# Kernel optimization log

Measured on AMD Instinct MI355X. Metric: run time of the kernel, lower is better.

The kernel has to match this reference:

```python
import jax, jax.numpy as jnp
import numpy as np

# Geometry constants hardcoded in the torch module
B, H, W = 1, 256, 256
A, DC = 64, 1024            # n_views, det_count
NSAMP = 512                  # samples per ray for the line integral
DSRC, DDET, SPACING = 500.0, 500.0, 2.0
NPAD = 2048                  # fft padding (next pow2 >= 2*DC)
FEAT = 32


def _bilinear_image(img, px, py):
    """Bilinear sample img (B,H,W) at centered coords px,py (any shape). Zero outside."""
    b, hh, ww = img.shape
    cx = px + (ww - 1) / 2.0
    cy = py + (hh - 1) / 2.0
    x0 = jnp.floor(cx); y0 = jnp.floor(cy)
    fx = cx - x0; fy = cy - y0
    x0i = x0.astype(jnp.int32); y0i = y0.astype(jnp.int32)
    flat = img.reshape(b, -1)

    def gather(yi, xi):
        valid = (yi >= 0) & (yi < hh) & (xi >= 0) & (xi < ww)
        yc = jnp.clip(yi, 0, hh - 1); xc = jnp.clip(xi, 0, ww - 1)
        idx = (yc * ww + xc).reshape(-1)
        v = jnp.take(flat, idx, axis=1).reshape((b,) + yi.shape)
        return v * valid.astype(img.dtype)

    return (gather(y0i, x0i) * (1 - fx) * (1 - fy)
            + gather(y0i, x0i + 1) * fx * (1 - fy)
            + gather(y0i + 1, x0i) * (1 - fx) * fy
            + gather(y0i + 1, x0i + 1) * fx * fy)


def fan_forward(img, theta):
    """Ray-driven fan-beam forward projection. img (B,1,H,W) -> sino (B,A,DC)."""
    im = img[:, 0]
    c = jnp.cos(theta); s = jnp.sin(theta)
    src = DSRC * jnp.stack([c, s], -1)                    # (A,2) source positions
    e = jnp.stack([-s, c], -1)                            # detector axis
    u = (jnp.arange(DC) - (DC - 1) / 2.0) * SPACING       # detector offsets
    det = -DDET * jnp.stack([c, s], -1)[:, None, :] + u[None, :, None] * e[:, None, :]  # (A,DC,2)
    d = det - src[:, None, :]
    L = jnp.sqrt(jnp.sum(d * d, axis=-1))                 # (A,DC) ray lengths
    t = (jnp.arange(NSAMP, dtype=jnp.float32) + 0.5) / NSAMP
    pts = src[:, None, None, :] + t[None, None, :, None] * d[:, :, None, :]  # (A,DC,N,2)
    vals = _bilinear_image(im, pts[..., 0], pts[..., 1])  # (B,A,DC,N)
    return jnp.sum(vals, axis=-1) * (L / NSAMP)[None]


def filter_sinogram(sino):
    """Ram-Lak ramp filtering along the detector axis with zero-padding."""
    f = jnp.abs(jnp.fft.rfftfreq(NPAD)).astype(jnp.float32)  # cycles/sample
    sf = jnp.fft.rfft(sino, n=NPAD, axis=-1) * (2.0 * f)
    return jnp.fft.irfft(sf, n=NPAD, axis=-1)[..., :DC].astype(sino.dtype)


def fan_backprojection(sino, theta):
    """Pixel-driven fan-beam backprojection. sino (B,A,DC) -> (B,1,H,W)."""
    xs = jnp.arange(W, dtype=jnp.float32) - (W - 1) / 2.0
    ys = jnp.arange(H, dtype=jnp.float32) - (H - 1) / 2.0
    gx, gy = jnp.meshgrid(xs, ys)                         # (H,W)
    c = jnp.cos(theta)[:, None, None]; s = jnp.sin(theta)[:, None, None]
    xr = gx[None] * c + gy[None] * s                      # (A,H,W) rotated coords
    yr = -gx[None] * s + gy[None] * c
    denom = DSRC - xr
    uu = yr * (DSRC + DDET) / denom                       # detector coordinate
    wgt = (DSRC * DSRC) / (denom * denom)                 # fan-beam distance weight
    iu = uu / SPACING + (DC - 1) / 2.0
    i0 = jnp.floor(iu); fr = iu - i0
    i0i = i0.astype(jnp.int32)
    aidx = jnp.arange(A)[:, None, None]
    b = sino.shape[0]
    flat = sino.reshape(b, -1)

    def g(ii):
        valid = (ii >= 0) & (ii < DC)
        ic = jnp.clip(ii, 0, DC - 1)
        idx = (aidx * DC + ic).reshape(-1)
        v = jnp.take(flat, idx, axis=1).reshape((b, A, H, W))
        return v * valid.astype(sino.dtype)

    vals = g(i0i) * (1 - fr) + g(i0i + 1) * fr            # (B,A,H,W)
    bp = jnp.sum(vals * wgt[None], axis=1) * (jnp.pi / A)
    return bp[:, None]


def conv(x, w):
    return jax.lax.conv_general_dilated(x, w, (1, 1), 'SAME',
                                        dimension_numbers=('NCHW', 'OIHW', 'NCHW'))


def setup_inputs():
    key = jax.random.key(0)
    ks = jax.random.split(key, 8)
    x = jax.random.normal(ks[0], (B, 1, H, W), jnp.float32)
    theta = jnp.arange(A, dtype=jnp.float32) * (2.0 * np.pi / A)
    sinogram = jax.random.normal(ks[1], (B, A, DC), jnp.float32)

    def xav(k, shape):
        fan_in = shape[1] * 9; fan_out = shape[0] * 9
        return jax.random.normal(k, shape, jnp.float32) * np.sqrt(2.0 / (fan_in + fan_out)).astype(np.float32)

    return {
        'x': x, 'theta': theta, 'sinogram': sinogram,
        'lambda_step': jnp.float32(0.5), 'soft_thr': jnp.float32(0.01),
        'conv1_forward': xav(ks[2], (FEAT, 1, 3, 3)),
        'conv2_forward': xav(ks[3], (FEAT, FEAT, 3, 3)),
        'conv1_backward': xav(ks[4], (FEAT, FEAT, 3, 3)),
        'conv2_backward': xav(ks[5], (1, FEAT, 3, 3)),
    }


def reference(x, theta, sinogram, lambda_step, soft_thr,
              conv1_forward, conv2_forward, conv1_backward, conv2_backward):
    sino_pred = fan_forward(x, theta)
    filtered = filter_sinogram(sino_pred)
    X_fbp = fan_backprojection(filtered - sinogram, theta)
    x_input = x - lambda_step * X_fbp
    h = jax.nn.relu(conv(x_input, conv1_forward))
    x_forward = conv(h, conv2_forward)
    hs = jnp.sign(x_forward) * jax.nn.relu(jnp.abs(x_forward) - soft_thr)
    x_pred = conv(jax.nn.relu(conv(hs, conv1_backward)), conv2_backward)
    x_est = conv(jax.nn.relu(conv(x_forward, conv1_backward)), conv2_backward)
    symloss = x_est - x_input
    return (x_pred, symloss)
```

## Files before the change

### kernel.cpp

```cpp
#include <hip/hip_runtime.h>

#define DEV_INLINE __device__ __forceinline__

#define PI_F 3.14159265358979323846f

#define H_OFF     0
#define SINO_OFF  2048
#define DIFF_OFF  67584
#define XIN_OFF   133120
#define WF2F_OFF  198656
#define WF1B_OFF  207872
#define WF2B_OFF  212480
#define BUFA_OFF  217088
#define BUFB_OFF  2314240

typedef short bf16x8 __attribute__((ext_vector_type(8)));
typedef float f32x4 __attribute__((ext_vector_type(4)));

union FragI4 { int4 i4; bf16x8 v; };
union I4U    { int4 i4; int i[4]; };

DEV_INLINE unsigned rne1(float a) {
  unsigned u = __float_as_uint(a);
  return (u + 0x7FFFu + ((u >> 16) & 1u)) >> 16;
}
DEV_INLINE int pack_rne(float a, float b) {
  return (int)(rne1(a) | (rne1(b) << 16));
}

__global__ __launch_bounds__(256) void setup_kernel(
    const float* __restrict__ sino_in, const float* __restrict__ w2f,
    const float* __restrict__ w1b, const float* __restrict__ w2b,
    const float* __restrict__ img,
    float* __restrict__ h, float* __restrict__ diff,
    int* __restrict__ wf2f, int* __restrict__ wf1b, int* __restrict__ wf2b,
    float4* __restrict__ quadP, float* __restrict__ x_input) {
  const int b = blockIdx.x;
  const int tid = threadIdx.x;
  if (b < 64) {
    __shared__ float hp[8][32];
    const int cell = tid & 31;
    const int kq = tid >> 5;
    const int n = b * 32 + cell;
    float ssum = 0.0f;
    const float ang_scale = PI_F / 1024.0f;
    for (int k = kq * 128; k < kq * 128 + 128; ++k) {
      int m = (k * n) & 2047;
      ssum += (float)k * __cosf((float)m * ang_scale);
    }
    hp[kq][cell] = ssum;
    __syncthreads();
    if (tid < 32) {
      float S = 0.0f;
      #pragma unroll
      for (int q = 0; q < 8; ++q) S += hp[q][tid];
      int nn = b * 32 + tid;
      float sgn = (nn & 1) ? -1.0f : 1.0f;
      h[nn] = (S * (1.0f / 512.0f) + sgn) * (1.0f / 2048.0f);
    }
  } else if (b < 320) {
    int idx = (b - 64) * 256 + tid;
    diff[idx] = -sino_in[idx];
  } else if (b < 356) {
    const bool second = (b >= 338);
    int idx = (b - (second ? 338 : 320)) * 256 + tid;
    int d = idx & 3;
    int L = (idx >> 2) & 63;
    int jm = idx >> 8;
    int j = jm >> 1, mt = jm & 1;
    int co = mt * 16 + (L & 15);
    int ci0 = (L >> 4) * 8 + 2 * d;
    const float* w = second ? w1b : w2f;
    int v = pack_rne(w[co * 288 + ci0 * 9 + j], w[co * 288 + (ci0 + 1) * 9 + j]);
    (second ? wf1b : wf2f)[idx] = v;
  } else if (b < 617) {
    int idx = (b - 356) * 256 + tid;
    if (idx < 258 * 258) {
      int y = idx / 258;
      int x = idx - y * 258;
      float4 v;
      int ay = y - 1, bx = x - 1;
      bool y0ok = (ay >= 0 && ay < 256);
      bool y1ok = (ay + 1 >= 0 && ay + 1 < 256);
      bool x0ok = (bx >= 0 && bx < 256);
      bool x1ok = (bx + 1 >= 0 && bx + 1 < 256);
      v.x = (y0ok && x0ok) ? img[(ay << 8) + bx] : 0.0f;
      v.y = (y0ok && x1ok) ? img[(ay << 8) + bx + 1] : 0.0f;
      v.z = (y1ok && x0ok) ? img[((ay + 1) << 8) + bx] : 0.0f;
      v.w = (y1ok && x1ok) ? img[((ay + 1) << 8) + bx + 1] : 0.0f;
      quadP[idx] = v;
    }
  } else if (b < 873) {
    int idx = (b - 617) * 256 + tid;
    x_input[idx] = img[idx];
  } else {
    int d = tid & 3;
    int L = tid >> 2;
    int n = L & 15;
    int k0 = (L >> 4) * 8 + 2 * d;
    float lo = (n < 9) ? w2b[k0 * 9 + n] : 0.0f;
    float hi = (n < 9) ? w2b[(k0 + 1) * 9 + n] : 0.0f;
    wf2b[tid] = pack_rne(lo, hi);
  }
}

__global__ __launch_bounds__(256) void fwdproj(
    const float4* __restrict__ quadP, const float* __restrict__ theta,
    float* __restrict__ sino) {
  __shared__ float part[8][32];
  __shared__ float cs[2];
  const int tid = threadIdx.x;
  const int a = blockIdx.x >> 5;
  const int cell = tid & 31;
  const int chunk = tid >> 5;
  const int d = ((blockIdx.x & 31) << 5) + cell;
  if (tid == 0) {
    float th = theta[a];
    cs[0] = cosf(th);
    cs[1] = sinf(th);
  }
  __syncthreads();
  const float c = cs[0], s = cs[1];
  const float u = ((float)d - 511.5f) * 2.0f;
  const float dxv = -1000.0f * c - u * s;
  const float dyv = -1000.0f * s + u * c;
  const float L = sqrtf(1.0e6f + u * u);
  const float sx = fmaf(500.0f, c, 127.5f);
  const float sy = fmaf(500.0f, s, 127.5f);

  float tlo = 0.0f, thi = 1.0f;
  if (fabsf(dxv) > 1e-6f) {
    float inv = 1.0f / dxv;
    float a0 = (-1.0f - sx) * inv, a1 = (256.0f - sx) * inv;
    tlo = fmaxf(tlo, fminf(a0, a1));
    thi = fminf(thi, fmaxf(a0, a1));
  } else if (sx <= -1.0f || sx >= 256.0f) {
    thi = -1.0f;
  }
  if (fabsf(dyv) > 1e-6f) {
    float inv = 1.0f / dyv;
    float a0 = (-1.0f - sy) * inv, a1 = (256.0f - sy) * inv;
    tlo = fmaxf(tlo, fminf(a0, a1));
    thi = fminf(thi, fmaxf(a0, a1));
  } else if (sy <= -1.0f || sy >= 256.0f) {
    thi = -1.0f;
  }
  int imin = (int)ceilf(tlo * 512.0f - 0.5f) - 1;
  imin = imin < 0 ? 0 : imin;
  int imax = (int)floorf(thi * 512.0f - 0.5f) + 1;
  imax = imax > 511 ? 511 : imax;

  float acc = 0.0f;
  for (int i = imin + chunk; i <= imax; i += 8) {
    float t = ((float)i + 0.5f) * (1.0f / 512.0f);
    float cx = fmaf(t, dxv, sx);
    float cy = fmaf(t, dyv, sy);
    cx = fminf(fmaxf(cx, -1.0f), 256.0f);
    cy = fminf(fmaxf(cy, -1.0f), 256.0f);
    float xf = floorf(cx), yf = floorf(cy);
    float fx = cx - xf, fy = cy - yf;
    int ix = (int)xf + 1;
    int iy = (int)yf + 1;
    float4 q = quadP[iy * 258 + ix];
    float gx = 1.0f - fx, gy = 1.0f - fy;
    acc += gy * (gx * q.x + fx * q.y) + fy * (gx * q.z + fx * q.w);
  }
  part[chunk][cell] = acc;
  __syncthreads();
  if (tid < 32) {
    float r = 0.0f;
    #pragma unroll
    for (int q = 0; q < 8; ++q) r += part[q][tid];
    sino[a * 1024 + ((blockIdx.x & 31) << 5) + tid] = r * (L * (1.0f / 512.0f));
  }
}

__global__ __launch_bounds__(256) void filt(
    const float* __restrict__ sino_pred, const float* __restrict__ h,
    float* __restrict__ diff) {
  __shared__ __align__(16) float srow[256];
  __shared__ __align__(16) float hext[4104];
  const int a = blockIdx.x >> 2;
  const int q = blockIdx.x & 3;
  const int tid = threadIdx.x;
  const int k0base = q * 256;
  srow[tid] = sino_pred[a * 1024 + k0base + tid];
  for (int n = tid; n < 4104; n += 256) hext[n] = h[(n - 2051) & 2047];
  __syncthreads();
  const int dd0 = tid * 4;
  float acc0 = 0.f, acc1 = 0.f, acc2 = 0.f, acc3 = 0.f;
  #pragma unroll 4
  for (int kk = 0; kk < 256; kk += 4) {
    float4 sv = *reinterpret_cast<const float4*>(&srow[kk]);
    int nb = dd0 + 2048 - k0base - kk;
    float4 hA = *reinterpret_cast<const float4*>(&hext[nb]);
    float4 hB = *reinterpret_cast<const float4*>(&hext[nb + 4]);
    acc0 = fmaf(sv.x, hA.w, acc0); acc0 = fmaf(sv.y, hA.z, acc0);
    acc0 = fmaf(sv.z, hA.y, acc0); acc0 = fmaf(sv.w, hA.x, acc0);
    acc1 = fmaf(sv.x, hB.x, acc1); acc1 = fmaf(sv.y, hA.w, acc1);
    acc1 = fmaf(sv.z, hA.z, acc1); acc1 = fmaf(sv.w, hA.y, acc1);
    acc2 = fmaf(sv.x, hB.y, acc2); acc2 = fmaf(sv.y, hB.x, acc2);
    acc2 = fmaf(sv.z, hA.w, acc2); acc2 = fmaf(sv.w, hA.z, acc2);
    acc3 = fmaf(sv.x, hB.z, acc3); acc3 = fmaf(sv.y, hB.y, acc3);
    acc3 = fmaf(sv.z, hB.x, acc3); acc3 = fmaf(sv.w, hA.w, acc3);
  }
  float* o = diff + a * 1024 + dd0;
  atomicAdd(o + 0, acc0);
  atomicAdd(o + 1, acc1);
  atomicAdd(o + 2, acc2);
  atomicAdd(o + 3, acc3);
}

__global__ __launch_bounds__(256) void backproj_part(
    const float* __restrict__ diff, const float* __restrict__ theta,
    const float* __restrict__ lam_p, float* __restrict__ x_input) {
  __shared__ float cst[16], snt[16];
  const int tid = threadIdx.x;
  const int tileb = blockIdx.x & 255;
  const int a0 = (blockIdx.x >> 8) << 4;
  if (tid < 16) {
    float th = theta[a0 + tid];
    cst[tid] = cosf(th);
    snt[tid] = sinf(th);
  }
  __syncthreads();
  const int tX = (tileb & 3) << 6;
  const int tY = (tileb >> 2) << 2;
  const int pxi = tX + (tid & 63);
  const int pyi = tY + (tid >> 6);
  const float gx = (float)pxi - 127.5f;
  const float gy = (float)pyi - 127.5f;
  float acc = 0.0f;
  for (int ai = 0; ai < 16; ++ai) {
    float c = cst[ai], s = snt[ai];
    float xr = gx * c + gy * s;
    float yr = gy * c - gx * s;
    float denom = 500.0f - xr;
    float inv = 1.0f / denom;
    float uu = yr * 1000.0f * inv;
    float wgt = 250000.0f * inv * inv;
    float iu = uu * 0.5f + 511.5f;
    float i0f = floorf(iu);
    float fr = iu - i0f;
    int i0 = (int)i0f;
    int c0 = min(max(i0, 0), 1023);
    int c1 = min(max(i0 + 1, 0), 1023);
    float m0 = (i0 >= 0 && i0 < 1024) ? 1.0f : 0.0f;
    float m1 = (i0 + 1 >= 0 && i0 + 1 < 1024) ? 1.0f : 0.0f;
    const float* row = diff + (a0 + ai) * 1024;
    float v0 = row[c0] * m0;
    float v1 = row[c1] * m1;
    acc += (v0 * (1.0f - fr) + v1 * fr) * wgt;
  }
  int p = (pyi << 8) + pxi;
  atomicAdd(x_input + p, -lam_p[0] * 0.04908738521234052f * acc);
}

__global__ __launch_bounds__(256) void conv12f(
    const float* __restrict__ x_input, const float* __restrict__ w1f,
    const int* __restrict__ wf2f, int* __restrict__ xfp) {
  __shared__ float xin[8][36];
  __shared__ __align__(16) int htile[3264];
  const int tid = threadIdx.x;
  const int lane = tid & 63;
  const int wave = tid >> 6;
  const int tX = (blockIdx.x & 7) << 5;
  const int tY = (blockIdx.x >> 3) << 2;

  FragI4 wf[2][9];
  const int4* wfg = (const int4*)wf2f;
  #pragma unroll
  for (int mt = 0; mt < 2; ++mt)
    #pragma unroll
    for (int j = 0; j < 9; ++j) wf[mt][j].i4 = wfg[(j * 2 + mt) * 64 + lane];

  for (int idx = tid; idx < 288; idx += 256) {
    int sy = idx / 36;
    int sx = idx - sy * 36;
    int gy = tY + sy - 2, gx = tX + sx - 2;
    xin[sy][sx] = (gy >= 0 && gy < 256 && gx >= 0 && gx < 256)
                      ? x_input[(gy << 8) + gx] : 0.0f;
  }
  __syncthreads();

  for (int pos = tid; pos < 204; pos += 256) {
    int yy = pos / 34;
    int xx = pos - yy * 34;
    int hy = tY + yy - 1, hx = tX + xx - 1;
    bool hin = (hy >= 0 && hy < 256 && hx >= 0 && hx < 256);
    float v[9];
    #pragma unroll
    for (int dy = 0; dy < 3; ++dy)
      #pragma unroll
      for (int dx = 0; dx < 3; ++dx) v[dy * 3 + dx] = xin[yy + dy][xx + dx];
    int packs[16];
    #pragma unroll
    for (int c2 = 0; c2 < 16; ++c2) {
      float r0 = 0.0f, r1 = 0.0f;
      #pragma unroll
      for (int j = 0; j < 9; ++j) {
        r0 = fmaf(v[j], w1f[(2 * c2) * 9 + j], r0);
        r1 = fmaf(v[j], w1f[(2 * c2 + 1) * 9 + j], r1);
      }
      r0 = hin ? fmaxf(r0, 0.0f) : 0.0f;
      r1 = hin ? fmaxf(r1, 0.0f) : 0.0f;
      packs[c2] = pack_rne(r0, r1);
    }
    #pragma unroll
    for (int g = 0; g < 4; ++g)
      *reinterpret_cast<int4*>(&htile[g * 816 + pos * 4]) =
          make_int4(packs[4 * g], packs[4 * g + 1],
                    packs[4 * g + 2], packs[4 * g + 3]);
  }
  __syncthreads();

  const int y = wave;
  const int n = lane & 15;
  const int q = lane >> 4;
  const int qb = q * 816;
  for (int xt = 0; xt < 2; ++xt) {
    const int x0 = xt << 4;
    f32x4 acc0 = {0.f, 0.f, 0.f, 0.f};
    f32x4 acc1 = {0.f, 0.f, 0.f, 0.f};
    #pragma unroll
    for (int j = 0; j < 9; ++j) {
      int dy = j / 3, dx = j - dy * 3;
      int pb = (y + dy) * 34 + x0 + dx + n;
      FragI4 bf;
      bf.i4 = *reinterpret_cast<const int4*>(&htile[qb + pb * 4]);
      acc0 = __builtin_amdgcn_mfma_f32_16x16x32_bf16(wf[0][j].v, bf.v, acc0, 0, 0, 0);
      acc1 = __builtin_amdgcn_mfma_f32_16x16x32_bf16(wf[1][j].v, bf.v, acc1, 0, 0, 0);
    }
    const int gpos = ((tY + y) << 8) + tX + x0 + n;
    int2* xp = (int2*)(xfp + (gpos << 4));
    xp[q]     = make_int2(pack_rne(acc0[0], acc0[1]), pack_rne(acc0[2], acc0[3]));
    xp[4 + q] = make_int2(pack_rne(acc1[0], acc1[1]), pack_rne(acc1[2], acc1[3]));
  }
}

__global__ __launch_bounds__(256) void branch_tail(
    const int* __restrict__ xfp, const int* __restrict__ wf1b,
    const int* __restrict__ wf2b, const float* __restrict__ thr_p,
    const float* __restrict__ x_input, float* __restrict__ out) {
  __shared__ __align__(16) int ldsX[8704];
  __shared__ __align__(16) int ldsD[6400];
  float* ldsP = (float*)ldsX;
  const int tid = threadIdx.x;
  const int lane = tid & 63;
  const int wave = tid >> 6;
  const int branch = blockIdx.x >> 8;
  const int tileb = blockIdx.x & 255;
  const int tX = (tileb & 3) << 6;
  const int tY = (tileb >> 2) << 2;
  const float thr = thr_p[0];
  const bool soft = (branch == 0);

  FragI4 wf[2][9];
  const int4* wfg = (const int4*)wf1b;
  #pragma unroll
  for (int mt = 0; mt < 2; ++mt)
    #pragma unroll
    for (int j = 0; j < 9; ++j) wf[mt][j].i4 = wfg[(j * 2 + mt) * 64 + lane];
  FragI4 wb;
  wb.i4 = ((const int4*)wf2b)[lane];

  if (tid < 16) {
    int g = tid >> 2, px = 396 + (tid & 3);
    *reinterpret_cast<int4*>(&ldsD[g * 1600 + px * 4]) = make_int4(0, 0, 0, 0);
  }

  #pragma unroll
  for (int t = 0; t < 3; ++t) {
    int p = tid + t * 256;
    if (p < 544) {
      int sy = p / 68;
      int sx = p - sy * 68;
      int gy = tY + sy - 2, gx = tX + sx - 2;
      bool ok = ((unsigned)gy < 256u) && ((unsigned)gx < 256u);
      I4U w[4];
      if (ok) {
        const int4* src = (const int4*)(xfp + (((gy << 8) + gx) << 4));
        w[0].i4 = src[0]; w[1].i4 = src[1]; w[2].i4 = src[2]; w[3].i4 = src[3];
      } else {
        w[0].i4 = w[1].i4 = w[2].i4 = w[3].i4 = make_int4(0, 0, 0, 0);
      }
      #pragma unroll
      for (int g = 0; g < 4; ++g) {
        if (soft) {
          #pragma unroll
          for (int k = 0; k < 4; ++k) {
            int v = w[g].i[k];
            float lo = __uint_as_float(((unsigned)v) << 16);
            float hi = __uint_as_float(((unsigned)v) & 0xFFFF0000u);
            lo = fmaxf(lo - thr, 0.0f) + fminf(lo + thr, 0.0f);
            hi = fmaxf(hi - thr, 0.0f) + fminf(hi + thr, 0.0f);
            w[g].i[k] = pack_rne(lo, hi);
          }
        }
        *reinterpret_cast<int4*>(&ldsX[g * 2176 + p * 4]) = w[g].i4;
      }
    }
  }
  __syncthreads();

  const int n = lane & 15;
  const int q = lane >> 4;
  const int rxtab[5] = {-1, 15, 31, 47, 49};
  for (int t = wave; t < 30; t += 4) {
    int trow = t / 5;
    int ry = trow - 1;
    int rx0 = rxtab[t - trow * 5];
    int rxn = rx0 + n;
    bool inimg = ((unsigned)(tX + rxn) < 256u) && ((unsigned)(tY + ry) < 256u);
    int pxD = (ry + 1) * 66 + rxn + 1;
    f32x4 acc0 = {0.f, 0.f, 0.f, 0.f};
    f32x4 acc1 = {0.f, 0.f, 0.f, 0.f};
    #pragma unroll
    for (int j = 0; j < 9; ++j) {
      int dy = j / 3, dx = j - dy * 3;
      int pb = (ry + 1 + dy) * 68 + rx0 + 1 + dx + n;
      FragI4 bf;
      bf.i4 = *reinterpret_cast<const int4*>(&ldsX[q * 2176 + pb * 4]);
      acc0 = __builtin_amdgcn_mfma_f32_16x16x32_bf16(wf[0][j].v, bf.v, acc0, 0, 0, 0);
      acc1 = __builtin_amdgcn_mfma_f32_16x16x32_bf16(wf[1][j].v, bf.v, acc1, 0, 0, 0);
    }
    float a00 = inimg ? fmaxf(acc0[0], 0.0f) : 0.0f;
    float a01 = inimg ? fmaxf(acc0[1], 0.0f) : 0.0f;
    float a02 = inimg ? fmaxf(acc0[2], 0.0f) : 0.0f;
    float a03 = inimg ? fmaxf(acc0[3], 0.0f) : 0.0f;
    float a10 = inimg ? fmaxf(acc1[0], 0.0f) : 0.0f;
    float a11 = inimg ? fmaxf(acc1[1], 0.0f) : 0.0f;
    float a12 = inimg ? fmaxf(acc1[2], 0.0f) : 0.0f;
    float a13 = inimg ? fmaxf(acc1[3], 0.0f) : 0.0f;
    *reinterpret_cast<int2*>(
        &ldsD[(q >> 1) * 1600 + pxD * 4 + (q & 1) * 2]) =
        make_int2(pack_rne(a00, a01), pack_rne(a02, a03));
    *reinterpret_cast<int2*>(
        &ldsD[(2 + (q >> 1)) * 1600 + pxD * 4 + (q & 1) * 2]) =
        make_int2(pack_rne(a10, a11), pack_rne(a12, a13));
  }
  __syncthreads();

  for (int t = wave; t < 25; t += 4) {
    int pbase = t << 4;
    FragI4 af;
    af.i4 = *reinterpret_cast<const int4*>(&ldsD[q * 1600 + (pbase + n) * 4]);
    f32x4 acc = {0.f, 0.f, 0.f, 0.f};
    acc = __builtin_amdgcn_mfma_f32_16x16x32_bf16(af.v, wb.v, acc, 0, 0, 0);
    #pragma unroll
    for (int r = 0; r < 4; ++r)
      ldsP[(pbase + q * 4 + r) * 17 + n] = acc[r];
  }
  __syncthreads();

  const int px = tid & 63, py = tid >> 6;
  float acc = 0.0f;
  #pragma unroll
  for (int j = 0; j < 9; ++j) {
    int dy = j / 3, dx = j - dy * 3;
    int rp = (py + dy) * 66 + px + dx;
    acc += ldsP[rp * 17 + j];
  }
  const int p = ((tY + py) << 8) + tX + px;
  if (branch == 0) out[p] = acc;
  else out[65536 + p] = acc - x_input[p];
}

extern "C" void kernel_launch(void* const* d_in, const int* in_sizes, int n_in,
                              void* d_out, int out_size, void* d_ws, size_t ws_size,
                              hipStream_t stream) {
  const float* x       = (const float*)d_in[0];
  const float* theta   = (const float*)d_in[1];
  const float* sino_in = (const float*)d_in[2];
  const float* lam     = (const float*)d_in[3];
  const float* thr     = (const float*)d_in[4];
  const float* w_c1f   = (const float*)d_in[5];
  const float* w_c2f   = (const float*)d_in[6];
  const float* w_c1b   = (const float*)d_in[7];
  const float* w_c2b   = (const float*)d_in[8];
  float* out = (float*)d_out;
  float* ws  = (float*)d_ws;

  float* h         = ws + H_OFF;
  float* sino_pred = ws + SINO_OFF;
  float* diff      = ws + DIFF_OFF;
  float* x_input   = ws + XIN_OFF;
  int*   wf2f      = (int*)(ws + WF2F_OFF);
  int*   wf1b      = (int*)(ws + WF1B_OFF);
  int*   wf2b      = (int*)(ws + WF2B_OFF);
  float4* quadP    = (float4*)(ws + BUFA_OFF);
  int*   xfp       = (int*)(ws + BUFB_OFF);

  setup_kernel<<<874, 256, 0, stream>>>(sino_in, w_c2f, w_c1b, w_c2b, x, h,
                                        diff, wf2f, wf1b, wf2b, quadP, x_input);
  fwdproj<<<2048, 256, 0, stream>>>(quadP, theta, sino_pred);
  filt<<<256, 256, 0, stream>>>(sino_pred, h, diff);
  backproj_part<<<1024, 256, 0, stream>>>(diff, theta, lam, x_input);
  conv12f<<<512, 256, 0, stream>>>(x_input, w_c1f, wf2f, xfp);
  branch_tail<<<512, 256, 0, stream>>>(xfp, wf1b, wf2b, thr, x_input, out);
}
```

Measured before the change: 127.4 us.

## Fuse x_input init into backprojection, shrink filter LUT, unroll forward projection loop

Backprojection now runs one 512-thread block per pixel tile covering all 64 views. It reduces the four angle-group partials in shared memory and writes x_input = img - lam*sum directly. This removes the setup copy blocks and the global atomics. The filter kernel loads only the 1288-entry window of the ramp kernel it needs instead of the full 4104-entry extension, cutting shared-memory fill work. The forward projector's sample loop is manually unrolled by two so both gathers can be issued before use, at the cost of more registers.

```diff
diff --git a/kernel.cpp b/kernel.cpp
--- a/kernel.cpp
+++ b/kernel.cpp
@@ -34,7 +34,7 @@
     const float* __restrict__ img,
     float* __restrict__ h, float* __restrict__ diff,
     int* __restrict__ wf2f, int* __restrict__ wf1b, int* __restrict__ wf2b,
-    float4* __restrict__ quadP, float* __restrict__ x_input) {
+    float4* __restrict__ quadP) {
   const int b = blockIdx.x;
   const int tid = threadIdx.x;
   if (b < 64) {
@@ -90,9 +90,6 @@
       v.w = (y1ok && x1ok) ? img[((ay + 1) << 8) + bx + 1] : 0.0f;
       quadP[idx] = v;
     }
-  } else if (b < 873) {
-    int idx = (b - 617) * 256 + tid;
-    x_input[idx] = img[idx];
   } else {
     int d = tid & 3;
     int L = tid >> 2;
@@ -151,7 +148,36 @@
   imax = imax > 511 ? 511 : imax;
 
   float acc = 0.0f;
-  for (int i = imin + chunk; i <= imax; i += 8) {
+  int i = imin + chunk;
+  for (; i + 8 <= imax; i += 16) {
+    float t0 = ((float)i + 0.5f) * (1.0f / 512.0f);
+    float cx0 = fmaf(t0, dxv, sx);
+    float cy0 = fmaf(t0, dyv, sy);
+    cx0 = fminf(fmaxf(cx0, -1.0f), 256.0f);
+    cy0 = fminf(fmaxf(cy0, -1.0f), 256.0f);
+    float xf0 = floorf(cx0), yf0 = floorf(cy0);
+    float fx0 = cx0 - xf0, fy0 = cy0 - yf0;
+    int idx0 = ((int)yf0 + 1) * 258 + (int)xf0 + 1;
+    float t1 = ((float)(i + 8) + 0.5f) * (1.0f / 512.0f);
+    float cx1 = fmaf(t1, dxv, sx);
+    float cy1 = fmaf(t1, dyv, sy);
+    cx1 = fminf(fmaxf(cx1, -1.0f), 256.0f);
+    cy1 = fminf(fmaxf(cy1, -1.0f), 256.0f);
+    float xf1 = floorf(cx1), yf1 = floorf(cy1);
+    float fx1 = cx1 - xf1, fy1 = cy1 - yf1;
+    int idx1 = ((int)yf1 + 1) * 258 + (int)xf1 + 1;
+    float4 q0 = quadP[idx0];
+    float4 q1 = quadP[idx1];
+    {
+      float gx = 1.0f - fx0, gy = 1.0f - fy0;
+      acc += gy * (gx * q0.x + fx0 * q0.y) + fy0 * (gx * q0.z + fx0 * q0.w);
+    }
+    {
+      float gx = 1.0f - fx1, gy = 1.0f - fy1;
+      acc += gy * (gx * q1.x + fx1 * q1.y) + fy1 * (gx * q1.z + fx1 * q1.w);
+    }
+  }
+  if (i <= imax) {
     float t = ((float)i + 0.5f) * (1.0f / 512.0f);
     float cx = fmaf(t, dxv, sx);
     float cy = fmaf(t, dyv, sy);
@@ -179,22 +205,23 @@
     const float* __restrict__ sino_pred, const float* __restrict__ h,
     float* __restrict__ diff) {
   __shared__ __align__(16) float srow[256];
-  __shared__ __align__(16) float hext[4104];
+  __shared__ __align__(16) float hextW[1288];
   const int a = blockIdx.x >> 2;
   const int q = blockIdx.x & 3;
   const int tid = threadIdx.x;
   const int k0base = q * 256;
   srow[tid] = sino_pred[a * 1024 + k0base + tid];
-  for (int n = tid; n < 4104; n += 256) hext[n] = h[(n - 2051) & 2047];
+  const int shift = 259 + k0base;
+  for (int m = tid; m < 1288; m += 256) hextW[m] = h[(m - shift) & 2047];
   __syncthreads();
   const int dd0 = tid * 4;
   float acc0 = 0.f, acc1 = 0.f, acc2 = 0.f, acc3 = 0.f;
   #pragma unroll 4
   for (int kk = 0; kk < 256; kk += 4) {
     float4 sv = *reinterpret_cast<const float4*>(&srow[kk]);
-    int nb = dd0 + 2048 - k0base - kk;
-    float4 hA = *reinterpret_cast<const float4*>(&hext[nb]);
-    float4 hB = *reinterpret_cast<const float4*>(&hext[nb + 4]);
+    int mb = dd0 + 256 - kk;
+    float4 hA = *reinterpret_cast<const float4*>(&hextW[mb]);
+    float4 hB = *reinterpret_cast<const float4*>(&hextW[mb + 4]);
     acc0 = fmaf(sv.x, hA.w, acc0); acc0 = fmaf(sv.y, hA.z, acc0);
     acc0 = fmaf(sv.z, hA.y, acc0); acc0 = fmaf(sv.w, hA.x, acc0);
     acc1 = fmaf(sv.x, hB.x, acc1); acc1 = fmaf(sv.y, hA.w, acc1);
@@ -211,27 +238,29 @@
   atomicAdd(o + 3, acc3);
 }
 
-__global__ __launch_bounds__(256) void backproj_part(
+__global__ __launch_bounds__(512) void backproj(
     const float* __restrict__ diff, const float* __restrict__ theta,
-    const float* __restrict__ lam_p, float* __restrict__ x_input) {
-  __shared__ float cst[16], snt[16];
+    const float* __restrict__ lam_p, const float* __restrict__ img,
+    float* __restrict__ x_input) {
+  __shared__ float cst[64], snt[64];
+  __shared__ float part[512];
   const int tid = threadIdx.x;
-  const int tileb = blockIdx.x & 255;
-  const int a0 = (blockIdx.x >> 8) << 4;
-  if (tid < 16) {
-    float th = theta[a0 + tid];
+  if (tid < 64) {
+    float th = theta[tid];
     cst[tid] = cosf(th);
     snt[tid] = sinf(th);
   }
   __syncthreads();
-  const int tX = (tileb & 3) << 6;
-  const int tY = (tileb >> 2) << 2;
-  const int pxi = tX + (tid & 63);
-  const int pyi = tY + (tid >> 6);
+  const int tX = (blockIdx.x & 7) << 5;
+  const int tY = (blockIdx.x >> 3) << 2;
+  const int pl = tid & 127;
+  const int ag = tid >> 7;
+  const int pxi = tX + (pl & 31);
+  const int pyi = tY + (pl >> 5);
   const float gx = (float)pxi - 127.5f;
   const float gy = (float)pyi - 127.5f;
   float acc = 0.0f;
-  for (int ai = 0; ai < 16; ++ai) {
+  for (int ai = ag * 16; ai < ag * 16 + 16; ++ai) {
     float c = cst[ai], s = snt[ai];
     float xr = gx * c + gy * s;
     float yr = gy * c - gx * s;
@@ -247,13 +276,18 @@
     int c1 = min(max(i0 + 1, 0), 1023);
     float m0 = (i0 >= 0 && i0 < 1024) ? 1.0f : 0.0f;
     float m1 = (i0 + 1 >= 0 && i0 + 1 < 1024) ? 1.0f : 0.0f;
-    const float* row = diff + (a0 + ai) * 1024;
+    const float* row = diff + ai * 1024;
     float v0 = row[c0] * m0;
     float v1 = row[c1] * m1;
     acc += (v0 * (1.0f - fr) + v1 * fr) * wgt;
   }
-  int p = (pyi << 8) + pxi;
-  atomicAdd(x_input + p, -lam_p[0] * 0.04908738521234052f * acc);
+  part[tid] = acc;
+  __syncthreads();
+  if (tid < 128) {
+    float sum = part[tid] + part[tid + 128] + part[tid + 256] + part[tid + 384];
+    int p = ((tY + (tid >> 5)) << 8) + tX + (tid & 31);
+    x_input[p] = img[p] - lam_p[0] * 0.04908738521234052f * sum;
+  }
 }
 
 __global__ __launch_bounds__(256) void conv12f(
@@ -491,11 +525,11 @@
   float4* quadP    = (float4*)(ws + BUFA_OFF);
   int*   xfp       = (int*)(ws + BUFB_OFF);
 
-  setup_kernel<<<874, 256, 0, stream>>>(sino_in, w_c2f, w_c1b, w_c2b, x, h,
-                                        diff, wf2f, wf1b, wf2b, quadP, x_input);
+  setup_kernel<<<618, 256, 0, stream>>>(sino_in, w_c2f, w_c1b, w_c2b, x, h,
+                                        diff, wf2f, wf1b, wf2b, quadP);
   fwdproj<<<2048, 256, 0, stream>>>(quadP, theta, sino_pred);
   filt<<<256, 256, 0, stream>>>(sino_pred, h, diff);
-  backproj_part<<<1024, 256, 0, stream>>>(diff, theta, lam, x_input);
+  backproj<<<512, 512, 0, stream>>>(diff, theta, lam, x, x_input);
   conv12f<<<512, 256, 0, stream>>>(x_input, w_c1f, wf2f, xfp);
   branch_tail<<<512, 256, 0, stream>>>(xfp, wf1b, wf2b, thr, x_input, out);
 }
```

After: 127.4 us (median of 2 runs). Within noise of the previous version (-0.0%).
